# Kernel tuning notes

Hardware: AMD Instinct MI355X
Metric: run time of the kernel (lower is better)

Reference implementation:

```python
import jax, jax.numpy as jnp
import numpy as np

B, T, S, A = 4, 10, 6, 6
HID, L, IMG = 512, 6, 128
NCH = 16  # spatial-softmax channels
_px, _py = np.meshgrid(np.linspace(-1.0, 1.0, IMG), np.linspace(-1.0, 1.0, IMG))
POSX = jnp.asarray(_px.reshape(-1), jnp.float32)
POSY = jnp.asarray(_py.reshape(-1), jnp.float32)


def _conv_relu(x, w, b):
    y = jax.lax.conv_general_dilated(x, w, (1, 1), 'SAME',
                                     dimension_numbers=('NCHW', 'OIHW', 'NCHW'))
    return jax.nn.relu(y + b[None, :, None, None])


def _cnn_ss(x, ws, bs):
    for w, b in zip(ws, bs):
        x = _conv_relu(x, w, b)
    n = x.shape[0]
    attn = jax.nn.softmax(x.reshape(n, NCH, -1), axis=-1)  # (n, 16, H*W)
    ex = attn @ POSX  # (n, 16)
    ey = attn @ POSY
    return jnp.stack([ex, ey], axis=-1).reshape(n, 2 * NCH)  # (n, 32)


def _lstm_cell(x, h, c, wih, whh, bih, bhh):
    g = x @ wih.T + bih + h @ whh.T + bhh
    i, f, gg, o = jnp.split(g, 4, axis=-1)  # torch LSTMCell gate order i,f,g,o
    c2 = jax.nn.sigmoid(f) * c + jax.nn.sigmoid(i) * jnp.tanh(gg)
    h2 = jax.nn.sigmoid(o) * jnp.tanh(c2)
    return h2, c2


def setup_inputs() -> dict:
    key = jax.random.key(0)
    ks = iter(jax.random.split(key, 64))

    def nrm(shape, s=0.05):
        return jax.random.normal(next(ks), shape, dtype=jnp.float32) * s

    inp = {
        'seq_img_main': nrm((B, T, 3, IMG, IMG), 1.0),
        'seq_img_secondary': nrm((B, T, 3, IMG, IMG), 1.0),
        'seq_states': nrm((B, T, S), 1.0),
    }
    chans = [(32, 3), (64, 32), (128, 64), (16, 128)]
    for cam in ('m', 's'):
        for j, (o, ci) in enumerate(chans):
            inp[f'{cam}_w{j}'] = nrm((o, ci, 3, 3))
            inp[f'{cam}_b{j}'] = nrm((o,))
    in0, inr = S + 64, HID + 64  # 70 and 576
    inp['wih0'] = nrm((4 * HID, in0)); inp['whh0'] = nrm((4 * HID, HID))
    inp['bih0'] = nrm((4 * HID,)); inp['bhh0'] = nrm((4 * HID,))
    inp['wih_r'] = nrm((L - 1, 4 * HID, inr)); inp['whh_r'] = nrm((L - 1, 4 * HID, HID))
    inp['bih_r'] = nrm((L - 1, 4 * HID)); inp['bhh_r'] = nrm((L - 1, 4 * HID))
    inp['out_w'] = nrm((A, inr)); inp['out_b'] = nrm((A,))
    return inp


def reference(seq_img_main, seq_img_secondary, seq_states,
              m_w0, m_b0, m_w1, m_b1, m_w2, m_b2, m_w3, m_b3,
              s_w0, s_b0, s_w1, s_b1, s_w2, s_b2, s_w3, s_b3,
              wih0, whh0, bih0, bhh0, wih_r, whh_r, bih_r, bhh_r,
              out_w, out_b):
    b, t = seq_img_main.shape[:2]
    fm = _cnn_ss(seq_img_main.reshape(b * t, 3, IMG, IMG),
                 [m_w0, m_w1, m_w2, m_w3], [m_b0, m_b1, m_b2, m_b3])
    fs = _cnn_ss(seq_img_secondary.reshape(b * t, 3, IMG, IMG),
                 [s_w0, s_w1, s_w2, s_w3], [s_b0, s_b1, s_b2, s_b3])
    img = jnp.concatenate([fm, fs], axis=-1).reshape(b, t, 64)  # (B,T,64)

    h0 = jnp.zeros((L, b, HID), jnp.float32)
    c0 = jnp.zeros((L, b, HID), jnp.float32)

    def step(carry, xt):
        h, c = carry
        st, im = xt  # (B,S), (B,64)
        x = jnp.concatenate([st, im], axis=-1)
        hn, cn = _lstm_cell(x, h[0], c[0], wih0, whh0, bih0, bhh0)
        hs, cs = [hn], [cn]
        for l in range(L - 1):
            x = jnp.concatenate([hs[-1], im], axis=-1)
            hl, cl = _lstm_cell(x, h[l + 1], c[l + 1],
                                wih_r[l], whh_r[l], bih_r[l], bhh_r[l])
            hs.append(hl); cs.append(cl)
        out = jnp.concatenate([hs[-1], im], axis=-1) @ out_w.T + out_b
        return (jnp.stack(hs), jnp.stack(cs)), out

    _, outs = jax.lax.scan(step, (h0, c0),
                           (seq_states.transpose(1, 0, 2), img.transpose(1, 0, 2)))
    return outs.transpose(1, 0, 2)  # (B,T,A)
```

## Files before the change

### kernel.cpp

```cpp
#include <hip/hip_runtime.h>
#include <hip/hip_bf16.h>
#include <math.h>

typedef __hip_bfloat16 bf16;
typedef short bf16x8 __attribute__((ext_vector_type(8)));
typedef float f32x4 __attribute__((ext_vector_type(4)));

static constexpr int HWPX = 16384;
static constexpr int NBL  = 64;

__device__ inline float sigmoidf_(float x) { return 1.0f / (1.0f + expf(-x)); }
__device__ inline float bflo(unsigned u) { return __uint_as_float(u << 16); }
__device__ inline float bfhi(unsigned u) { return __uint_as_float(u & 0xffff0000u); }
__device__ inline int swz(int x) { return (x ^ (x >> 2)) & 3; }

__device__ inline void gll16(const bf16* g, short* l) {
    __builtin_amdgcn_global_load_lds(
        (const __attribute__((address_space(1))) void*)g,
        (__attribute__((address_space(3))) void*)l, 16, 0, 0);
}

__device__ inline int flag_ld(const int* p) {
    return __hip_atomic_load(p, __ATOMIC_RELAXED, __HIP_MEMORY_SCOPE_AGENT);
}
__device__ inline void flag_st(int* p, int v) {
    __hip_atomic_store(p, v, __ATOMIC_RELAXED, __HIP_MEMORY_SCOPE_AGENT);
}
__device__ inline float devload(const float* p) {
    return __hip_atomic_load(p, __ATOMIC_RELAXED, __HIP_MEMORY_SCOPE_AGENT);
}
__device__ inline unsigned long long devload2(const float* p) {
    return __hip_atomic_load((const unsigned long long*)p,
                             __ATOMIC_RELAXED, __HIP_MEMORY_SCOPE_AGENT);
}
__device__ inline void devstore(float* p, float v) {
    __hip_atomic_store(p, v, __ATOMIC_RELAXED, __HIP_MEMORY_SCOPE_AGENT);
}

__global__ __launch_bounds__(256) void prep_lstm_k(
    const float* __restrict__ wih0, const float* __restrict__ whh0,
    const float* __restrict__ wihr, const float* __restrict__ whhr,
    bf16* __restrict__ d0, bf16* __restrict__ d1,
    bf16* __restrict__ d2, bf16* __restrict__ d3)
{
    const size_t nA = 2048ull * 72, nB = 2048ull * 512;
    const size_t nC = 5ull * 2048 * 576, nD = 5ull * 2048 * 512;
    for (size_t i = blockIdx.x * 256ull + threadIdx.x; i < nA + nB + nC + nD;
         i += (size_t)gridDim.x * 256) {
        if (i < nA) {
            int c = (int)(i % 72), r = (int)(i / 72);
            d0[i] = __float2bfloat16(c < 70 ? wih0[(size_t)r * 70 + c] : 0.f);
        } else if (i < nA + nB) {
            size_t k = i - nA; d1[k] = __float2bfloat16(whh0[k]);
        } else if (i < nA + nB + nC) {
            size_t k = i - nA - nB; d2[k] = __float2bfloat16(wihr[k]);
        } else {
            size_t k = i - nA - nB - nC; d3[k] = __float2bfloat16(whhr[k]);
        }
    }
}

struct ConvW {
    const float* src[8];
    bf16* dst[8];
};

__global__ __launch_bounds__(256) void prep_conv_k(ConvW a)
{
    const int sizes[4] = {3072, 18432, 73728, 18432};
    const int cins[4] = {3, 32, 64, 128};
    const int couts[4] = {32, 64, 128, 16};
    int total = 2 * 113664;
    for (int idx = blockIdx.x * 256 + threadIdx.x; idx < total; idx += gridDim.x * 256) {
        int i = idx, cam = 0;
        if (i >= 113664) { cam = 1; i -= 113664; }
        int layer = 0;
        while (layer < 3 && i >= sizes[layer]) { i -= sizes[layer]; ++layer; }
        const float* w = a.src[cam * 4 + layer];
        bf16* d = a.dst[cam * 4 + layer];
        if (layer == 0) {
            int k = i & 31, co = (i >> 5) & 31, ky = i >> 10;
            int kx = k >> 3, c = k & 7;
            float v = (kx < 3 && c < 3) ? w[((co * 3 + c) * 3 + ky) * 3 + kx] : 0.f;
            d[i] = __float2bfloat16(v);
        } else {
            int CIN = cins[layer], COUT = couts[layer], KC = CIN / 32;
            int e = i & 7;
            int t2 = i >> 3;
            int co = t2 % COUT;
            int t3 = t2 / COUT;
            int q = t3 & 3;
            int t4 = t3 >> 2;
            int kc = t4 % KC;
            int tap = t4 / KC;
            d[i] = __float2bfloat16(w[((size_t)(co * CIN + kc * 32 + q * 8 + e)) * 9 + tap]);
        }
    }
}

__global__ __launch_bounds__(256) void conv0_nhwc(
    const float* __restrict__ srcm, const float* __restrict__ srcs,
    const bf16* __restrict__ w0m, const bf16* __restrict__ w0s,
    const float* __restrict__ bm, const float* __restrict__ bs,
    bf16* __restrict__ out, int c0)
{
    const int y = blockIdx.x;
    const int cam = blockIdx.y;
    const int img = blockIdx.z;
    const int ci_ = cam * gridDim.z + img;
    const float* inImg = (cam ? srcs : srcm) + (size_t)(c0 + img) * 3 * HWPX;
    const bf16* wT0 = cam ? w0s : w0m;
    const float* bias = cam ? bs : bm;
    const int tid = threadIdx.x;
    const int wave = tid >> 6, lane = tid & 63;
    const int wm = wave & 1, wn = wave >> 1;
    const int q = lane >> 4, n16 = lane & 15;

    __shared__ short smem[3 * 130 * 16];

    for (int d = tid; d < 3 * 130; d += 256) {
        int x = d % 130, r = d / 130;
        int yy = y + r - 1, xx = x - 1;
        bf16 v8[8];
#pragma unroll
        for (int c = 0; c < 8; ++c) v8[c] = __float2bfloat16(0.f);
        if ((unsigned)yy < 128u && (unsigned)xx < 128u) {
            int o = yy * 128 + xx;
            v8[0] = __float2bfloat16(inImg[o]);
            v8[1] = __float2bfloat16(inImg[HWPX + o]);
            v8[2] = __float2bfloat16(inImg[2 * HWPX + o]);
        }
        *(bf16x8*)(void*)&smem[(r * 130 + x) * 16] = *(bf16x8*)(void*)v8;
        *(bf16x8*)(void*)&smem[(r * 130 + x) * 16 + 8] = (bf16x8)0;
    }
    __syncthreads();

    f32x4 acc[4];
#pragma unroll
    for (int nt = 0; nt < 4; ++nt) acc[nt] = f32x4{0.f, 0.f, 0.f, 0.f};

    const int co = wm * 16 + n16;
#pragma unroll
    for (int ky = 0; ky < 3; ++ky) {
        bf16x8 aF = *(const bf16x8*)(const void*)(wT0 + ((size_t)(ky * 32 + co) * 32) + q * 8);
#pragma unroll
        for (int nt = 0; nt < 4; ++nt) {
            int x = (wn * 4 + nt) * 16 + n16;
            int off = (q < 3) ? (ky * 130 + x + q) * 16 : (ky * 130 + x) * 16 + 8;
            bf16x8 bF = *(const bf16x8*)(const void*)&smem[off];
            acc[nt] = __builtin_amdgcn_mfma_f32_16x16x32_bf16(aF, bF, acc[nt], 0, 0, 0);
        }
    }

    int co0 = wm * 16 + q * 4;
#pragma unroll
    for (int nt = 0; nt < 4; ++nt) {
        int x = (wn * 4 + nt) * 16 + n16;
        bf16 tmp[4];
#pragma unroll
        for (int r = 0; r < 4; ++r) {
            float v = acc[nt][r] + bias[co0 + r];
            tmp[r] = __float2bfloat16(v > 0.f ? v : 0.f);
        }
        *reinterpret_cast<uint2*>(out + ((size_t)ci_ * HWPX + y * 128 + x) * 32 + co0)
            = *reinterpret_cast<uint2*>(tmp);
    }
}

template <int CIN, int COUT>
__global__ __launch_bounds__(256, 4) void conv2r(
    const bf16* __restrict__ in, const bf16* __restrict__ wTm,
    const bf16* __restrict__ wTs, const float* __restrict__ bm,
    const float* __restrict__ bs, bf16* __restrict__ out,
    const char* __restrict__ zpage)
{
    constexpr int KC = CIN / 32;
    constexpr int NB = (KC > 1) ? 2 : 1;
    constexpr int MW = COUT / 32;
    constexpr int SLOTS = 4 * 264;

    const int y0 = (blockIdx.x >> 1) * 2;
    const int x0 = (blockIdx.x & 1) * 64;
    const int cam = blockIdx.y;
    const int img = blockIdx.z;
    const int ci_ = cam * gridDim.z + img;
    const bf16* wT = cam ? wTs : wTm;
    const float* bias = cam ? bs : bm;
    const int tid = threadIdx.x;
    const int wave = tid >> 6, lane = tid & 63;
    const int wrow = wave >> 1, wm = wave & 1;
    const int q = lane >> 4, n16 = lane & 15;

    __shared__ short smem[NB][SLOTS * 8];
    const bf16* inImg = in + (size_t)ci_ * HWPX * CIN;

    const bf16* sptr[5];
#pragma unroll
    for (int it = 0; it < 5; ++it) {
        int s = it * 256 + tid;
        int r = s / 264, s2 = s - r * 264;
        int sx = s2 >> 2;
        int g = (s2 & 3) ^ swz(sx);
        int yy = y0 + r - 1, xx = x0 + sx - 1;
        bool ok = (s < SLOTS) && ((unsigned)yy < 128u) && ((unsigned)xx < 128u);
        sptr[it] = ok ? inImg + ((size_t)yy * 128 + xx) * CIN + g * 8
                      : (const bf16*)(zpage + (tid & 255) * 16);
    }
    auto stage = [&](int kc, int buf) {
#pragma unroll
        for (int it = 0; it < 5; ++it) {
            if (it * 256 + tid < SLOTS)
                gll16(sptr[it] + kc * 32, &smem[buf][it * 2048 + wave * 512]);
        }
    };

    f32x4 acc[MW][4];
#pragma unroll
    for (int mt = 0; mt < MW; ++mt)
#pragma unroll
        for (int nt = 0; nt < 4; ++nt) acc[mt][nt] = f32x4{0.f, 0.f, 0.f, 0.f};

    stage(0, 0);
    for (int kc = 0; kc < KC; ++kc) {
        __syncthreads();
        if (kc + 1 < KC) stage(kc + 1, (kc + 1) % NB);
        const short* sb = smem[kc % NB];
#pragma unroll
        for (int ky = 0; ky < 3; ++ky) {
#pragma unroll
            for (int kx = 0; kx < 3; ++kx) {
                bf16x8 aF[MW];
#pragma unroll
                for (int mt = 0; mt < MW; ++mt) {
                    int co = (wm * MW + mt) * 16 + n16;
                    aF[mt] = *(const bf16x8*)(const void*)(wT +
                        ((((size_t)(ky * 3 + kx) * KC + kc) * 4 + q) * COUT + co) * 8);
                }
#pragma unroll
                for (int nt = 0; nt < 4; ++nt) {
                    int xt = nt * 16 + n16 + kx;
                    int slot = (wrow + ky) * 264 + xt * 4 + (q ^ swz(xt));
                    bf16x8 bF = *(const bf16x8*)(const void*)&sb[slot * 8];
#pragma unroll
                    for (int mt = 0; mt < MW; ++mt)
                        acc[mt][nt] = __builtin_amdgcn_mfma_f32_16x16x32_bf16(
                            aF[mt], bF, acc[mt][nt], 0, 0, 0);
                }
            }
        }
    }

    const int y = y0 + wrow;
#pragma unroll
    for (int mt = 0; mt < MW; ++mt) {
        int co0 = (wm * MW + mt) * 16 + q * 4;
#pragma unroll
        for (int nt = 0; nt < 4; ++nt) {
            int x = x0 + nt * 16 + n16;
            bf16 tmp[4];
#pragma unroll
            for (int r = 0; r < 4; ++r) {
                float v = acc[mt][nt][r] + bias[co0 + r];
                tmp[r] = __float2bfloat16(v > 0.f ? v : 0.f);
            }
            *reinterpret_cast<uint2*>(out + ((size_t)ci_ * HWPX + y * 128 + x) * COUT + co0)
                = *reinterpret_cast<uint2*>(tmp);
        }
    }
}

__global__ __launch_bounds__(256, 6) void conv4_xs(
    const bf16* __restrict__ in, const bf16* __restrict__ wTm,
    const bf16* __restrict__ wTs, const float* __restrict__ bm,
    const float* __restrict__ bs,
    float* __restrict__ partial,
    const char* __restrict__ zpage, int c0)
{
    constexpr int CIN = 128, COUT = 16, KC = 4;
    constexpr int SLOTS = 3 * 66 * 4;
    const int y = blockIdx.x >> 1;
    const int xh = blockIdx.x & 1;
    const int x0 = xh * 64;
    const int cam = blockIdx.y;
    const int img = blockIdx.z;
    const int ci_ = cam * gridDim.z + img;
    const int gimg = cam * 40 + c0 + img;
    const bf16* wT = cam ? wTs : wTm;
    const float* bias = cam ? bs : bm;
    const int tid = threadIdx.x;
    const int wave = tid >> 6, lane = tid & 63;
    const int q = lane >> 4, n16 = lane & 15;

    __shared__ short smem[2][SLOTS * 8];
    __shared__ float sred[3][4][16];
    const bf16* inImg = in + (size_t)ci_ * HWPX * CIN;

    const bf16* sptr[4];
#pragma unroll
    for (int it = 0; it < 4; ++it) {
        int s = it * 256 + tid;
        int r = s / 264, s2 = s - r * 264;
        int sx = s2 >> 2;
        int g = (s2 & 3) ^ swz(sx);
        int yy = y + r - 1, xx = x0 + sx - 1;
        bool ok = (s < SLOTS) && ((unsigned)yy < 128u) && ((unsigned)xx < 128u);
        sptr[it] = ok ? inImg + ((size_t)yy * 128 + xx) * CIN + g * 8
                      : (const bf16*)(zpage + (tid & 255) * 16);
    }
    auto stage = [&](int kc, int buf) {
#pragma unroll
        for (int it = 0; it < 4; ++it) {
            if (it * 256 + tid < SLOTS)
                gll16(sptr[it] + kc * 32, &smem[buf][it * 2048 + wave * 512]);
        }
    };

    f32x4 acc = f32x4{0.f, 0.f, 0.f, 0.f};

    stage(0, 0);
    for (int kc = 0; kc < KC; ++kc) {
        __syncthreads();
        if (kc + 1 < KC) stage(kc + 1, (kc + 1) & 1);
        const short* sb = smem[kc & 1];
#pragma unroll
        for (int ky = 0; ky < 3; ++ky) {
#pragma unroll
            for (int kx = 0; kx < 3; ++kx) {
                bf16x8 aF = *(const bf16x8*)(const void*)(wT +
                    ((((size_t)(ky * 3 + kx) * KC + kc) * 4 + q) * COUT + n16) * 8);
                int xt = wave * 16 + n16 + kx;
                int slot = xt * 4 + (q ^ swz(xt));
                bf16x8 bF = *(const bf16x8*)(const void*)&sb[ky * 2112 + slot * 8];
                acc = __builtin_amdgcn_mfma_f32_16x16x32_bf16(aF, bF, acc, 0, 0, 0);
            }
        }
    }

    float v[4];
    int x = x0 + wave * 16 + n16;
    float px = -1.f + (2.f / 127.f) * x;
#pragma unroll
    for (int r = 0; r < 4; ++r) {
        float t = acc[r] + bias[q * 4 + r];
        v[r] = t > 0.f ? t : 0.f;
    }
    float M[4];
#pragma unroll
    for (int r = 0; r < 4; ++r) {
        M[r] = v[r];
        M[r] = fmaxf(M[r], __shfl_xor(M[r], 1));
        M[r] = fmaxf(M[r], __shfl_xor(M[r], 2));
        M[r] = fmaxf(M[r], __shfl_xor(M[r], 4));
        M[r] = fmaxf(M[r], __shfl_xor(M[r], 8));
    }
    if (n16 == 0)
#pragma unroll
        for (int r = 0; r < 4; ++r) sred[0][wave][q * 4 + r] = M[r];
    __syncthreads();
#pragma unroll
    for (int r = 0; r < 4; ++r) {
        M[r] = fmaxf(fmaxf(sred[0][0][q * 4 + r], sred[0][1][q * 4 + r]),
                     fmaxf(sred[0][2][q * 4 + r], sred[0][3][q * 4 + r]));
    }
    float s[4], sx[4];
#pragma unroll
    for (int r = 0; r < 4; ++r) {
        float e = expf(v[r] - M[r]);
        s[r] = e; sx[r] = e * px;
        s[r] += __shfl_xor(s[r], 1);  sx[r] += __shfl_xor(sx[r], 1);
        s[r] += __shfl_xor(s[r], 2);  sx[r] += __shfl_xor(sx[r], 2);
        s[r] += __shfl_xor(s[r], 4);  sx[r] += __shfl_xor(sx[r], 4);
        s[r] += __shfl_xor(s[r], 8);  sx[r] += __shfl_xor(sx[r], 8);
    }
    __syncthreads();
    if (n16 == 0)
#pragma unroll
        for (int r = 0; r < 4; ++r) {
            sred[1][wave][q * 4 + r] = s[r];
            sred[2][wave][q * 4 + r] = sx[r];
        }
    __syncthreads();
    if (tid < 16) {
        float S = sred[1][0][tid] + sred[1][1][tid] + sred[1][2][tid] + sred[1][3][tid];
        float SX = sred[2][0][tid] + sred[2][1][tid] + sred[2][2][tid] + sred[2][3][tid];
        float Mv = fmaxf(fmaxf(sred[0][0][tid], sred[0][1][tid]),
                         fmaxf(sred[0][2][tid], sred[0][3][tid]));
        float* pp = partial + (((size_t)gimg * 16 + tid) * 256 + (y * 2 + xh)) * 4;
        pp[0] = Mv; pp[1] = S; pp[2] = SX;
    }
}

__global__ __launch_bounds__(256) void ssmerge_k(
    const float* __restrict__ partial, float* __restrict__ featm,
    float* __restrict__ feats)
{
    const int img = blockIdx.x;
    const int cam = img / 40, li = img % 40;
    float* feat = cam ? feats : featm;
    const int tid = threadIdx.x;
    const int co = tid >> 4, s = tid & 15;
    const float* base = partial + ((size_t)img * 16 + co) * 256 * 4;
    float M = -1e30f, S = 0.f, SX = 0.f, SY = 0.f;
    for (int i = s; i < 256; i += 16) {
        float m = base[i * 4], sv = base[i * 4 + 1], sxv = base[i * 4 + 2];
        float py = -1.f + (2.f / 127.f) * (i >> 1);
        float Mn = fmaxf(M, m);
        float w0 = expf(M - Mn), w1 = expf(m - Mn);
        S = S * w0 + sv * w1;
        SX = SX * w0 + sxv * w1;
        SY = SY * w0 + sv * py * w1;
        M = Mn;
    }
#pragma unroll
    for (int mask = 1; mask < 16; mask <<= 1) {
        float Mo = __shfl_xor(M, mask), So = __shfl_xor(S, mask);
        float SXo = __shfl_xor(SX, mask), SYo = __shfl_xor(SY, mask);
        float Mn = fmaxf(M, Mo);
        float w0 = expf(M - Mn), w1 = expf(Mo - Mn);
        S = S * w0 + So * w1; SX = SX * w0 + SXo * w1; SY = SY * w0 + SYo * w1;
        M = Mn;
    }
    if (s == 0) {
        feat[(size_t)li * 32 + 2 * co] = SX / S;
        feat[(size_t)li * 32 + 2 * co + 1] = SY / S;
    }
}

__device__ inline float imgfeat(const float* featm, const float* feats,
                                int b, int t, int k)
{
    int idx = (b * 10 + t) * 32;
    return k < 32 ? featm[idx + k] : feats[idx + k - 32];
}

__global__ __launch_bounds__(256) void lstm_pipe_k(
    const bf16* __restrict__ wih0p, const bf16* __restrict__ whh0b,
    const bf16* __restrict__ wihrb, const bf16* __restrict__ whhrb,
    const float* __restrict__ bih0, const float* __restrict__ bhh0,
    const float* __restrict__ bihr, const float* __restrict__ bhhr,
    const float* __restrict__ states,
    const float* __restrict__ featm, const float* __restrict__ feats,
    float* __restrict__ hAll, float* __restrict__ cAll,
    const float* __restrict__ out_w, const float* __restrict__ out_b,
    float* __restrict__ out, int* __restrict__ fl)
{
    const int gb = blockIdx.x;
    const int tid = threadIdx.x;

    if (gb == 6 * NBL) {
        for (int t = 0; t < 10; ++t) {
            if (tid < 64) {
                while (flag_ld(&fl[5 * 64 + tid]) < t + 1)
                    __builtin_amdgcn_s_sleep(1);
            }
            __syncthreads();
            const float* h5 = hAll + ((size_t)(t + 1) * 6 + 5) * 2048;
            int p = tid >> 3, sub = tid & 7;
            if (p < 24) {
                int b = p / 6, a = p % 6;
                const float* wr = out_w + a * 576;
                float acc = 0.f;
                for (int k = sub; k < 256; k += 8) {
                    union { unsigned long long u; float f[2]; } cv;
                    cv.u = devload2(&h5[b * 512 + k * 2]);
                    acc += wr[k * 2] * cv.f[0] + wr[k * 2 + 1] * cv.f[1];
                }
                for (int k = sub; k < 64; k += 8)
                    acc += wr[512 + k] * imgfeat(featm, feats, b, t, k);
                acc += __shfl_xor(acc, 1);
                acc += __shfl_xor(acc, 2);
                acc += __shfl_xor(acc, 4);
                if (sub == 0) out[(b * 10 + t) * 6 + a] = acc + out_b[a];
            }
        }
        return;
    }

    const int l = gb / NBL;
    const int bx = gb % NBL;

    const bf16 *wih, *whh;
    const float *bih, *bhh;
    int K1;
    if (l == 0) { wih = wih0p; whh = whh0b; bih = bih0; bhh = bhh0; K1 = 72; }
    else {
        wih = wihrb + (size_t)(l - 1) * 2048 * 576;
        whh = whhrb + (size_t)(l - 1) * 2048 * 512;
        bih = bihr + (l - 1) * 2048;
        bhh = bhhr + (l - 1) * 2048;
        K1 = 576;
    }
    const int XS = K1 + 512;
    float* cst = cAll + (size_t)l * 2048;

    const int b = tid >> 6;
    const int lane = tid & 63;
    const int jloc = lane >> 3;
    const int sub = lane & 7;
    const int j = bx * 8 + jloc;
    const int nb1 = K1 >> 3;

    __shared__ float xs[4 * 1088];

    for (int t = 0; t < 10; ++t) {
        if (l > 0 && tid < 64) {
            while (flag_ld(&fl[(l - 1) * 64 + tid]) < t + 1)
                __builtin_amdgcn_s_sleep(1);
        }
        if (t > 0 && tid >= 64 && tid < 128) {
            while (flag_ld(&fl[l * 64 + (tid - 64)]) < t)
                __builtin_amdgcn_s_sleep(1);
        }
        __syncthreads();

        const float* hprev = (l == 0) ? nullptr
                           : hAll + ((size_t)(t + 1) * 6 + (l - 1)) * 2048;
        const float* hold  = hAll + ((size_t)t * 6 + l) * 2048;
        float* hnew        = hAll + ((size_t)(t + 1) * 6 + l) * 2048;

        if (l > 0) {
            for (int i = tid; i < 4 * 512; i += 256) {
                int bb = i >> 9, kk = i & 511;
                union { unsigned long long u; float f[2]; } cv;
                int base;
                if (kk < 256) { cv.u = devload2(&hprev[bb * 512 + kk * 2]); base = bb * XS + kk * 2; }
                else { cv.u = devload2(&hold[bb * 512 + (kk - 256) * 2]); base = bb * XS + 576 + (kk - 256) * 2; }
                xs[base] = cv.f[0]; xs[base + 1] = cv.f[1];
            }
            if (tid < 256) {
                int bb = tid >> 6, k = tid & 63;
                xs[bb * XS + 512 + k] = imgfeat(featm, feats, bb, t, k);
            }
        } else {
            for (int i = tid; i < 4 * 256; i += 256) {
                int bb = i >> 8, kk = i & 255;
                union { unsigned long long u; float f[2]; } cv;
                cv.u = devload2(&hold[bb * 512 + kk * 2]);
                int base = bb * XS + 72 + kk * 2;
                xs[base] = cv.f[0]; xs[base + 1] = cv.f[1];
            }
            for (int i = tid; i < 4 * 72; i += 256) {
                int bb = i / 72, k = i - bb * 72;
                float v = (k < 6) ? states[(bb * 10 + t) * 6 + k]
                                  : (k < 70 ? imgfeat(featm, feats, bb, t, k - 6) : 0.f);
                xs[bb * XS + k] = v;
            }
        }
        __syncthreads();

        const float* xb = xs + b * XS;
        const float* hp = xb + K1;
        float dg[4] = {0.f, 0.f, 0.f, 0.f};
#pragma unroll
        for (int r = 0; r < 4; ++r) {
            const uint4* w1 = reinterpret_cast<const uint4*>(wih + (size_t)(j + r * 512) * K1);
            for (int g = sub; g < nb1; g += 8) {
                uint4 u = w1[g]; const float* xp = xb + g * 8;
                dg[r] += bflo(u.x) * xp[0] + bfhi(u.x) * xp[1] + bflo(u.y) * xp[2] + bfhi(u.y) * xp[3]
                       + bflo(u.z) * xp[4] + bfhi(u.z) * xp[5] + bflo(u.w) * xp[6] + bfhi(u.w) * xp[7];
            }
            const uint4* w2 = reinterpret_cast<const uint4*>(whh + (size_t)(j + r * 512) * 512);
            for (int g = sub; g < 64; g += 8) {
                uint4 u = w2[g]; const float* xp = hp + g * 8;
                dg[r] += bflo(u.x) * xp[0] + bfhi(u.x) * xp[1] + bflo(u.y) * xp[2] + bfhi(u.y) * xp[3]
                       + bflo(u.z) * xp[4] + bfhi(u.z) * xp[5] + bflo(u.w) * xp[6] + bfhi(u.w) * xp[7];
            }
        }
#pragma unroll
        for (int r = 0; r < 4; ++r) {
            dg[r] += __shfl_xor(dg[r], 1);
            dg[r] += __shfl_xor(dg[r], 2);
            dg[r] += __shfl_xor(dg[r], 4);
        }
        if (sub == 0) {
            float gi = dg[0] + bih[j] + bhh[j];
            float gf = dg[1] + bih[j + 512] + bhh[j + 512];
            float gg = dg[2] + bih[j + 1024] + bhh[j + 1024];
            float go = dg[3] + bih[j + 1536] + bhh[j + 1536];
            float cp = cst[b * 512 + j];
            float c2 = sigmoidf_(gf) * cp + sigmoidf_(gi) * tanhf(gg);
            float h2 = sigmoidf_(go) * tanhf(c2);
            cst[b * 512 + j] = c2;
            devstore(&hnew[b * 512 + j], h2);
        }
        __syncthreads();
        if (tid == 0) flag_st(&fl[l * 64 + bx], t + 1);
    }
}

extern "C" void kernel_launch(void* const* d_in, const int* in_sizes, int n_in,
                              void* d_out, int out_size, void* d_ws, size_t ws_size,
                              hipStream_t stream)
{
    const float* seq_m = (const float*)d_in[0];
    const float* seq_s = (const float*)d_in[1];
    const float* states = (const float*)d_in[2];
    const float *cw[2][4], *cb[2][4];
    for (int cam = 0; cam < 2; ++cam)
        for (int j = 0; j < 4; ++j) {
            cw[cam][j] = (const float*)d_in[3 + cam * 8 + j * 2];
            cb[cam][j] = (const float*)d_in[3 + cam * 8 + j * 2 + 1];
        }
    const float* wih0  = (const float*)d_in[19];
    const float* whh0  = (const float*)d_in[20];
    const float* bih0  = (const float*)d_in[21];
    const float* bhh0  = (const float*)d_in[22];
    const float* wih_r = (const float*)d_in[23];
    const float* whh_r = (const float*)d_in[24];
    const float* bih_r = (const float*)d_in[25];
    const float* bhh_r = (const float*)d_in[26];
    const float* out_w = (const float*)d_in[27];
    const float* out_b = (const float*)d_in[28];
    float* out = (float*)d_out;

    char* wsc = (char*)d_ws;
    auto carve = [&](size_t bytes) {
        char* p = wsc;
        wsc += (bytes + 255) & ~(size_t)255;
        return p;
    };
    float* featm = (float*)carve(40 * 32 * 4);
    float* feats = (float*)carve(40 * 32 * 4);
    float* hAll  = (float*)carve((size_t)11 * 6 * 2048 * 4);
    float* cAll  = (float*)carve((size_t)6 * 2048 * 4);
    char*  zpage = carve(8192);
    int*   lcnt  = (int*)carve((size_t)6 * 64 * 4);
    float* partial = (float*)carve((size_t)80 * 16 * 256 * 4 * 4);
    const int wtElts[4] = {3072, 18432, 73728, 18432};
    bf16* wT[2][4];
    for (int cam = 0; cam < 2; ++cam)
        for (int j = 0; j < 4; ++j) wT[cam][j] = (bf16*)carve(wtElts[j] * 2);
    bf16* wih0p = (bf16*)carve((size_t)2048 * 72 * 2);
    bf16* whh0b = (bf16*)carve((size_t)2048 * 512 * 2);
    bf16* wihrb = (bf16*)carve((size_t)5 * 2048 * 576 * 2);
    bf16* whhrb = (bf16*)carve((size_t)5 * 2048 * 512 * 2);

    size_t used = (size_t)(wsc - (char*)d_ws);
    size_t rem = ws_size > used ? ws_size - used : 0;
    int CHI = 1;
    const int cands[7] = {20, 10, 8, 5, 4, 2, 1};
    for (int i = 0; i < 7; ++i) {
        size_t need = (size_t)2 * cands[i] * (128 + 64) * HWPX * 2;
        if (need <= rem) { CHI = cands[i]; break; }
    }
    bf16* bufA = (bf16*)carve((size_t)2 * CHI * HWPX * 128 * 2);
    bf16* bufB = (bf16*)carve((size_t)2 * CHI * HWPX * 64 * 2);

    hipMemsetAsync(hAll, 0, 6 * 2048 * 4, stream);
    hipMemsetAsync(cAll, 0, 6 * 2048 * 4, stream);
    hipMemsetAsync(zpage, 0, 8192, stream);
    hipMemsetAsync(lcnt, 0, 6 * 64 * 4, stream);

    prep_lstm_k<<<2048, 256, 0, stream>>>(wih0, whh0, wih_r, whh_r,
                                          wih0p, whh0b, wihrb, whhrb);
    ConvW cwArg;
    for (int cam = 0; cam < 2; ++cam)
        for (int j = 0; j < 4; ++j) {
            cwArg.src[cam * 4 + j] = cw[cam][j];
            cwArg.dst[cam * 4 + j] = wT[cam][j];
        }
    prep_conv_k<<<888, 256, 0, stream>>>(cwArg);

    for (int c0 = 0; c0 < 40; c0 += CHI) {
        int ch = (40 - c0) < CHI ? (40 - c0) : CHI;
        conv0_nhwc<<<dim3(128, 2, ch), 256, 0, stream>>>(
            seq_m, seq_s, wT[0][0], wT[1][0], cb[0][0], cb[1][0], bufA, c0);
        conv2r<32, 64><<<dim3(128, 2, ch), 256, 0, stream>>>(
            bufA, wT[0][1], wT[1][1], cb[0][1], cb[1][1], bufB, zpage);
        conv2r<64, 128><<<dim3(128, 2, ch), 256, 0, stream>>>(
            bufB, wT[0][2], wT[1][2], cb[0][2], cb[1][2], bufA, zpage);
        conv4_xs<<<dim3(256, 2, ch), 256, 0, stream>>>(
            bufA, wT[0][3], wT[1][3], cb[0][3], cb[1][3], partial, zpage, c0);
    }
    ssmerge_k<<<80, 256, 0, stream>>>(partial, featm, feats);

    lstm_pipe_k<<<dim3(6 * NBL + 1), 256, 0, stream>>>(
        wih0p, whh0b, wihrb, whhrb, bih0, bhh0, bih_r, bhh_r,
        states, featm, feats, hAll, cAll, out_w, out_b, out, lcnt);
}
```

Baseline: 1.234 ms.

## Restructure LSTM pipeline: fewer blocks, each thread handles all batches, prefetch weights

Cuts the per-layer block count from 64 to 16. Each block now covers 32 hidden units, and each thread accumulates all 4 batch rows, so every weight load is reused across the batch instead of being reloaded per batch. Before the time loop, the block reads its weights once to warm the cache (an XOR into an unused register), and the layer loop is templated on K1 so the inner loops are fully unrolled. The aim is to cut redundant weight traffic and flag polling. The cost is less parallelism per layer and more register pressure from the 16 accumulators.

```diff
diff --git a/kernel.cpp b/kernel.cpp
--- a/kernel.cpp
+++ b/kernel.cpp
@@ -7,7 +7,7 @@
 typedef float f32x4 __attribute__((ext_vector_type(4)));
 
 static constexpr int HWPX = 16384;
-static constexpr int NBL  = 64;
+static constexpr int NBL  = 16;
 
 __device__ inline float sigmoidf_(float x) { return 1.0f / (1.0f + expf(-x)); }
 __device__ inline float bflo(unsigned u) { return __uint_as_float(u << 16); }
@@ -25,9 +25,6 @@
 }
 __device__ inline void flag_st(int* p, int v) {
     __hip_atomic_store(p, v, __ATOMIC_RELAXED, __HIP_MEMORY_SCOPE_AGENT);
-}
-__device__ inline float devload(const float* p) {
-    return __hip_atomic_load(p, __ATOMIC_RELAXED, __HIP_MEMORY_SCOPE_AGENT);
 }
 __device__ inline unsigned long long devload2(const float* p) {
     return __hip_atomic_load((const unsigned long long*)p,
@@ -433,6 +430,150 @@
     return k < 32 ? featm[idx + k] : feats[idx + k - 32];
 }
 
+template <int NB1>
+__device__ inline void cell_mm(const bf16* __restrict__ wih,
+                               const bf16* __restrict__ whh,
+                               const float* __restrict__ xs0,
+                               int j, int sub, float (&dg)[4][4])
+{
+    constexpr int K1 = NB1 * 8;
+    constexpr int XS = K1 + 512;
+#pragma unroll
+    for (int r = 0; r < 4; ++r) {
+        const uint4* __restrict__ w1 =
+            reinterpret_cast<const uint4*>(wih + (size_t)(j + r * 512) * K1);
+#pragma unroll
+        for (int g0 = 0; g0 < NB1; g0 += 8) {
+            int g = g0 + sub;
+            if (g0 + 7 < NB1 || g < NB1) {
+                uint4 u = w1[g];
+                float a0 = bflo(u.x), a1 = bfhi(u.x), a2 = bflo(u.y), a3 = bfhi(u.y);
+                float a4 = bflo(u.z), a5 = bfhi(u.z), a6 = bflo(u.w), a7 = bfhi(u.w);
+#pragma unroll
+                for (int b = 0; b < 4; ++b) {
+                    const float* xp = xs0 + b * XS + g * 8;
+                    dg[r][b] += a0 * xp[0] + a1 * xp[1] + a2 * xp[2] + a3 * xp[3]
+                              + a4 * xp[4] + a5 * xp[5] + a6 * xp[6] + a7 * xp[7];
+                }
+            }
+        }
+        const uint4* __restrict__ w2 =
+            reinterpret_cast<const uint4*>(whh + (size_t)(j + r * 512) * 512);
+#pragma unroll
+        for (int gi = 0; gi < 8; ++gi) {
+            int g = gi * 8 + sub;
+            uint4 u = w2[g];
+            float a0 = bflo(u.x), a1 = bfhi(u.x), a2 = bflo(u.y), a3 = bfhi(u.y);
+            float a4 = bflo(u.z), a5 = bfhi(u.z), a6 = bflo(u.w), a7 = bfhi(u.w);
+#pragma unroll
+            for (int b = 0; b < 4; ++b) {
+                const float* xp = xs0 + b * XS + K1 + g * 8;
+                dg[r][b] += a0 * xp[0] + a1 * xp[1] + a2 * xp[2] + a3 * xp[3]
+                          + a4 * xp[4] + a5 * xp[5] + a6 * xp[6] + a7 * xp[7];
+            }
+        }
+    }
+}
+
+template <int NB1>
+__device__ inline void lstm_layer_loop(
+    int l, int bx,
+    const bf16* __restrict__ wih, const bf16* __restrict__ whh,
+    const float* __restrict__ bih, const float* __restrict__ bhh,
+    const float* __restrict__ states,
+    const float* __restrict__ featm, const float* __restrict__ feats,
+    float* __restrict__ hAll, float* __restrict__ cst,
+    int* __restrict__ fl, float* __restrict__ xs)
+{
+    constexpr int K1 = NB1 * 8;
+    constexpr int XS = K1 + 512;
+    const int tid = threadIdx.x;
+    const int jloc = tid >> 3;
+    const int sub = tid & 7;
+    const int j = bx * 32 + jloc;
+
+    for (int t = 0; t < 10; ++t) {
+        if (l > 0 && tid < 16) {
+            while (flag_ld(&fl[(l - 1) * 16 + tid]) < t + 1)
+                __builtin_amdgcn_s_sleep(1);
+        }
+        if (t > 0 && tid >= 64 && tid < 80) {
+            while (flag_ld(&fl[l * 16 + (tid - 64)]) < t)
+                __builtin_amdgcn_s_sleep(1);
+        }
+        __syncthreads();
+
+        const float* hprev = (l == 0) ? nullptr
+                           : hAll + ((size_t)(t + 1) * 6 + (l - 1)) * 2048;
+        const float* hold  = hAll + ((size_t)t * 6 + l) * 2048;
+        float* hnew        = hAll + ((size_t)(t + 1) * 6 + l) * 2048;
+
+        if (NB1 == 72) {
+            for (int i = tid; i < 4 * 512; i += 256) {
+                int bb = i >> 9, kk = i & 511;
+                union { unsigned long long u; float f[2]; } cv;
+                int base;
+                if (kk < 256) { cv.u = devload2(&hprev[bb * 512 + kk * 2]); base = bb * XS + kk * 2; }
+                else { cv.u = devload2(&hold[bb * 512 + (kk - 256) * 2]); base = bb * XS + 576 + (kk - 256) * 2; }
+                xs[base] = cv.f[0]; xs[base + 1] = cv.f[1];
+            }
+            {
+                int bb = tid >> 6, k = tid & 63;
+                xs[bb * XS + 512 + k] = imgfeat(featm, feats, bb, t, k);
+            }
+        } else {
+            for (int i = tid; i < 4 * 256; i += 256) {
+                int bb = i >> 8, kk = i & 255;
+                union { unsigned long long u; float f[2]; } cv;
+                cv.u = devload2(&hold[bb * 512 + kk * 2]);
+                int base = bb * XS + 72 + kk * 2;
+                xs[base] = cv.f[0]; xs[base + 1] = cv.f[1];
+            }
+            for (int i = tid; i < 4 * 72; i += 256) {
+                int bb = i / 72, k = i - bb * 72;
+                float v = (k < 6) ? states[(bb * 10 + t) * 6 + k]
+                                  : (k < 70 ? imgfeat(featm, feats, bb, t, k - 6) : 0.f);
+                xs[bb * XS + k] = v;
+            }
+        }
+        __syncthreads();
+
+        float dg[4][4] = {{0.f, 0.f, 0.f, 0.f}, {0.f, 0.f, 0.f, 0.f},
+                          {0.f, 0.f, 0.f, 0.f}, {0.f, 0.f, 0.f, 0.f}};
+        cell_mm<NB1>(wih, whh, xs, j, sub, dg);
+
+#pragma unroll
+        for (int r = 0; r < 4; ++r)
+#pragma unroll
+            for (int b = 0; b < 4; ++b) {
+                dg[r][b] += __shfl_xor(dg[r][b], 1);
+                dg[r][b] += __shfl_xor(dg[r][b], 2);
+                dg[r][b] += __shfl_xor(dg[r][b], 4);
+            }
+
+        if (sub == 0) {
+            float b0 = bih[j] + bhh[j];
+            float b1 = bih[j + 512] + bhh[j + 512];
+            float b2 = bih[j + 1024] + bhh[j + 1024];
+            float b3 = bih[j + 1536] + bhh[j + 1536];
+#pragma unroll
+            for (int b = 0; b < 4; ++b) {
+                float gi = dg[0][b] + b0;
+                float gf = dg[1][b] + b1;
+                float gg = dg[2][b] + b2;
+                float go = dg[3][b] + b3;
+                float cp = cst[b * 512 + j];
+                float c2 = sigmoidf_(gf) * cp + sigmoidf_(gi) * tanhf(gg);
+                float h2 = sigmoidf_(go) * tanhf(c2);
+                cst[b * 512 + j] = c2;
+                devstore(&hnew[b * 512 + j], h2);
+            }
+        }
+        __syncthreads();
+        if (tid == 0) flag_st(&fl[l * 16 + bx], t + 1);
+    }
+}
+
 __global__ __launch_bounds__(256) void lstm_pipe_k(
     const bf16* __restrict__ wih0p, const bf16* __restrict__ whh0b,
     const bf16* __restrict__ wihrb, const bf16* __restrict__ whhrb,
@@ -446,11 +587,12 @@
 {
     const int gb = blockIdx.x;
     const int tid = threadIdx.x;
+    __shared__ float xs[4 * 1088];
 
     if (gb == 6 * NBL) {
         for (int t = 0; t < 10; ++t) {
-            if (tid < 64) {
-                while (flag_ld(&fl[5 * 64 + tid]) < t + 1)
+            if (tid < 16) {
+                while (flag_ld(&fl[5 * 16 + tid]) < t + 1)
                     __builtin_amdgcn_s_sleep(1);
             }
             __syncthreads();
@@ -472,6 +614,7 @@
                 acc += __shfl_xor(acc, 4);
                 if (sub == 0) out[(b * 10 + t) * 6 + a] = acc + out_b[a];
             }
+            __syncthreads();
         }
         return;
     }
@@ -481,111 +624,34 @@
 
     const bf16 *wih, *whh;
     const float *bih, *bhh;
-    int K1;
-    if (l == 0) { wih = wih0p; whh = whh0b; bih = bih0; bhh = bhh0; K1 = 72; }
+    if (l == 0) { wih = wih0p; whh = whh0b; bih = bih0; bhh = bhh0; }
     else {
         wih = wihrb + (size_t)(l - 1) * 2048 * 576;
         whh = whhrb + (size_t)(l - 1) * 2048 * 512;
         bih = bihr + (l - 1) * 2048;
         bhh = bhhr + (l - 1) * 2048;
-        K1 = 576;
-    }
-    const int XS = K1 + 512;
+    }
     float* cst = cAll + (size_t)l * 2048;
 
-    const int b = tid >> 6;
-    const int lane = tid & 63;
-    const int jloc = lane >> 3;
-    const int sub = lane & 7;
-    const int j = bx * 8 + jloc;
-    const int nb1 = K1 >> 3;
-
-    __shared__ float xs[4 * 1088];
-
-    for (int t = 0; t < 10; ++t) {
-        if (l > 0 && tid < 64) {
-            while (flag_ld(&fl[(l - 1) * 64 + tid]) < t + 1)
-                __builtin_amdgcn_s_sleep(1);
-        }
-        if (t > 0 && tid >= 64 && tid < 128) {
-            while (flag_ld(&fl[l * 64 + (tid - 64)]) < t)
-                __builtin_amdgcn_s_sleep(1);
-        }
-        __syncthreads();
-
-        const float* hprev = (l == 0) ? nullptr
-                           : hAll + ((size_t)(t + 1) * 6 + (l - 1)) * 2048;
-        const float* hold  = hAll + ((size_t)t * 6 + l) * 2048;
-        float* hnew        = hAll + ((size_t)(t + 1) * 6 + l) * 2048;
-
-        if (l > 0) {
-            for (int i = tid; i < 4 * 512; i += 256) {
-                int bb = i >> 9, kk = i & 511;
-                union { unsigned long long u; float f[2]; } cv;
-                int base;
-                if (kk < 256) { cv.u = devload2(&hprev[bb * 512 + kk * 2]); base = bb * XS + kk * 2; }
-                else { cv.u = devload2(&hold[bb * 512 + (kk - 256) * 2]); base = bb * XS + 576 + (kk - 256) * 2; }
-                xs[base] = cv.f[0]; xs[base + 1] = cv.f[1];
-            }
-            if (tid < 256) {
-                int bb = tid >> 6, k = tid & 63;
-                xs[bb * XS + 512 + k] = imgfeat(featm, feats, bb, t, k);
-            }
-        } else {
-            for (int i = tid; i < 4 * 256; i += 256) {
-                int bb = i >> 8, kk = i & 255;
-                union { unsigned long long u; float f[2]; } cv;
-                cv.u = devload2(&hold[bb * 512 + kk * 2]);
-                int base = bb * XS + 72 + kk * 2;
-                xs[base] = cv.f[0]; xs[base + 1] = cv.f[1];
-            }
-            for (int i = tid; i < 4 * 72; i += 256) {
-                int bb = i / 72, k = i - bb * 72;
-                float v = (k < 6) ? states[(bb * 10 + t) * 6 + k]
-                                  : (k < 70 ? imgfeat(featm, feats, bb, t, k - 6) : 0.f);
-                xs[bb * XS + k] = v;
-            }
-        }
-        __syncthreads();
-
-        const float* xb = xs + b * XS;
-        const float* hp = xb + K1;
-        float dg[4] = {0.f, 0.f, 0.f, 0.f};
-#pragma unroll
+    if (l > 0) {
+        const int jloc = tid >> 3, sub = tid & 7;
+        const int j = bx * 32 + jloc;
+        unsigned wsum = 0;
         for (int r = 0; r < 4; ++r) {
-            const uint4* w1 = reinterpret_cast<const uint4*>(wih + (size_t)(j + r * 512) * K1);
-            for (int g = sub; g < nb1; g += 8) {
-                uint4 u = w1[g]; const float* xp = xb + g * 8;
-                dg[r] += bflo(u.x) * xp[0] + bfhi(u.x) * xp[1] + bflo(u.y) * xp[2] + bfhi(u.y) * xp[3]
-                       + bflo(u.z) * xp[4] + bfhi(u.z) * xp[5] + bflo(u.w) * xp[6] + bfhi(u.w) * xp[7];
-            }
+            const uint4* w1 = reinterpret_cast<const uint4*>(wih + (size_t)(j + r * 512) * 576);
+            for (int g = sub; g < 72; g += 8) { uint4 u = w1[g]; wsum ^= u.x ^ u.w; }
             const uint4* w2 = reinterpret_cast<const uint4*>(whh + (size_t)(j + r * 512) * 512);
-            for (int g = sub; g < 64; g += 8) {
-                uint4 u = w2[g]; const float* xp = hp + g * 8;
-                dg[r] += bflo(u.x) * xp[0] + bfhi(u.x) * xp[1] + bflo(u.y) * xp[2] + bfhi(u.y) * xp[3]
-                       + bflo(u.z) * xp[4] + bfhi(u.z) * xp[5] + bflo(u.w) * xp[6] + bfhi(u.w) * xp[7];
-            }
-        }
-#pragma unroll
-        for (int r = 0; r < 4; ++r) {
-            dg[r] += __shfl_xor(dg[r], 1);
-            dg[r] += __shfl_xor(dg[r], 2);
-            dg[r] += __shfl_xor(dg[r], 4);
-        }
-        if (sub == 0) {
-            float gi = dg[0] + bih[j] + bhh[j];
-            float gf = dg[1] + bih[j + 512] + bhh[j + 512];
-            float gg = dg[2] + bih[j + 1024] + bhh[j + 1024];
-            float go = dg[3] + bih[j + 1536] + bhh[j + 1536];
-            float cp = cst[b * 512 + j];
-            float c2 = sigmoidf_(gf) * cp + sigmoidf_(gi) * tanhf(gg);
-            float h2 = sigmoidf_(go) * tanhf(c2);
-            cst[b * 512 + j] = c2;
-            devstore(&hnew[b * 512 + j], h2);
-        }
-        __syncthreads();
-        if (tid == 0) flag_st(&fl[l * 64 + bx], t + 1);
-    }
+            for (int g = sub; g < 64; g += 8) { uint4 u = w2[g]; wsum ^= u.x ^ u.w; }
+        }
+        asm volatile("" :: "v"(wsum));
+    }
+
+    if (l == 0)
+        lstm_layer_loop<9>(l, bx, wih, whh, bih, bhh, states, featm, feats,
+                           hAll, cst, fl, xs);
+    else
+        lstm_layer_loop<72>(l, bx, wih, whh, bih, bhh, states, featm, feats,
+                            hAll, cst, fl, xs);
 }
 
 extern "C" void kernel_launch(void* const* d_in, const int* in_sizes, int n_in,
@@ -624,7 +690,7 @@
     float* hAll  = (float*)carve((size_t)11 * 6 * 2048 * 4);
     float* cAll  = (float*)carve((size_t)6 * 2048 * 4);
     char*  zpage = carve(8192);
-    int*   lcnt  = (int*)carve((size_t)6 * 64 * 4);
+    int*   lcnt  = (int*)carve((size_t)6 * NBL * 4);
     float* partial = (float*)carve((size_t)80 * 16 * 256 * 4 * 4);
     const int wtElts[4] = {3072, 18432, 73728, 18432};
     bf16* wT[2][4];
@@ -649,7 +715,7 @@
     hipMemsetAsync(hAll, 0, 6 * 2048 * 4, stream);
     hipMemsetAsync(cAll, 0, 6 * 2048 * 4, stream);
     hipMemsetAsync(zpage, 0, 8192, stream);
-    hipMemsetAsync(lcnt, 0, 6 * 64 * 4, stream);
+    hipMemsetAsync(lcnt, 0, 6 * NBL * 4, stream);
 
     prep_lstm_k<<<2048, 256, 0, stream>>>(wih0, whh0, wih_r, whh_r,
                                           wih0p, whh0b, wihrb, whhrb);
```

New measurement: 1.238 ms. Within noise of the previous version (+0.4%).
